# Kernel tuning notes

Hardware: AMD Instinct MI355X
Metric: run time of the kernel (lower is better)

The kernel has to match this reference:

```python
import jax, jax.numpy as jnp
import numpy as np

B, N, D_MODEL = 2, 4096, 2048
H = 4
KEY_DIM = 1024          # d_model * 0.5
DK = KEY_DIM // H       # 256, head_qk_dim
DV = D_MODEL // H       # 512, head_v_dim
CHUNK = 64
EPS = 1e-5


def setup_inputs() -> dict:
    key = jax.random.key(0)
    ks = jax.random.split(key, 6)
    s = 0.02  # small init scale, mimics xavier-ish magnitude
    return {
        "x": jax.random.normal(ks[0], (B, N, D_MODEL), jnp.float32),
        "Wq": jax.random.normal(ks[1], (KEY_DIM, D_MODEL), jnp.float32) * s,
        "Wk": jax.random.normal(ks[2], (KEY_DIM, D_MODEL), jnp.float32) * s,
        "Wv": jax.random.normal(ks[3], (D_MODEL, D_MODEL), jnp.float32) * s,
        "Wg": jax.random.normal(ks[4], (D_MODEL, D_MODEL), jnp.float32) * s,
        "Wo": jax.random.normal(ks[5], (D_MODEL, D_MODEL), jnp.float32) * s,
        "gnorm_w": jnp.ones((DV,), jnp.float32),
    }


def _rope(qk):
    # non-interleaved rotary over full head dim; qk: [b, n, h, d]
    n, d = qk.shape[1], qk.shape[3]
    inv_freq = 1.0 / (10000.0 ** (jnp.arange(0, d, 2, dtype=jnp.float32) / d))
    freqs = jnp.arange(n, dtype=jnp.float32)[:, None] * inv_freq[None, :]  # [n, d/2]
    cos = jnp.cos(freqs)[None, :, None, :]
    sin = jnp.sin(freqs)[None, :, None, :]
    x1, x2 = qk[..., : d // 2], qk[..., d // 2 :]
    return jnp.concatenate([x1 * cos - x2 * sin, x2 * cos + x1 * sin], axis=-1)


def _retention_forward(x, Wq, Wk, Wv, Wg, Wo, gnorm_w):
    b, n, dm = x.shape
    dk, dv = Wq.shape[0] // H, Wv.shape[0] // H
    q = (x @ Wq.T).reshape(b, n, H, dk)
    k = (x @ Wk.T).reshape(b, n, H, dk)
    q, k = _rope(q), _rope(k)
    v = (x @ Wv.T).reshape(b, n, H, dv)
    # -> [b, h, n, d]
    q = q.transpose(0, 2, 1, 3) * (dk ** -0.5)
    k = k.transpose(0, 2, 1, 3)
    v = v.transpose(0, 2, 1, 3)

    # multi-scale decay: gamma_h = 1 - 2^(-5-h)
    gamma = 1.0 - jnp.exp2(-5.0 - jnp.arange(H, dtype=jnp.float32))  # [H]

    C = CHUNK
    nc = n // C
    qc = q.reshape(b, H, nc, C, dk).transpose(2, 0, 1, 3, 4)  # [nc,b,H,C,dk]
    kc = k.reshape(b, H, nc, C, dk).transpose(2, 0, 1, 3, 4)
    vc = v.reshape(b, H, nc, C, dv).transpose(2, 0, 1, 3, 4)

    i = jnp.arange(C)
    expo = (i[:, None] - i[None, :]).astype(jnp.float32)          # i - j
    dmask = jnp.where(expo >= 0, gamma[:, None, None] ** expo, 0.0)  # [H,C,C]
    g_in = gamma[:, None] ** (i + 1).astype(jnp.float32)          # [H,C] cross-chunk decay
    g_k = gamma[:, None] ** (C - 1 - i).astype(jnp.float32)       # [H,C] state-update decay
    g_C = gamma ** C                                               # [H]

    def step(S, inp):
        qi, ki, vi = inp  # [b,H,C,dk], [b,H,C,dk], [b,H,C,dv]
        attn = jnp.einsum('bhid,bhjd->bhij', qi, ki) * dmask[None]
        o_intra = jnp.einsum('bhij,bhjv->bhiv', attn, vi)
        o_inter = jnp.einsum('bhid,bhdv->bhiv', qi, S) * g_in[None, :, :, None]
        S_new = S * g_C[None, :, None, None] + jnp.einsum(
            'bhjd,bhjv->bhdv', ki * g_k[None, :, :, None], vi)
        return S_new, o_intra + o_inter

    S0 = jnp.zeros((b, H, dk, dv), x.dtype)
    _, oc = jax.lax.scan(step, S0, (qc, kc, vc))          # oc: [nc,b,H,C,dv]
    o = oc.transpose(1, 0, 3, 2, 4).reshape(b, n, H, dv)  # [b,n,h,dv]

    # per-head RMSNorm (group_norm over head_v_dim)
    o = o * jax.lax.rsqrt(jnp.mean(o * o, axis=-1, keepdims=True) + EPS) * gnorm_w

    g = jax.nn.silu(x @ Wg.T)  # [b,n,d_model]
    return (o.reshape(b, n, H * dv) * g) @ Wo.T


def reference(x, Wq, Wk, Wv, Wg, Wo, gnorm_w):
    return _retention_forward(x, Wq, Wk, Wv, Wg, Wo, gnorm_w)
```

## Files before the change

### kernel.cpp

```cpp
#include <hip/hip_runtime.h>
#include <hip/hip_bf16.h>
#include <stdint.h>

constexpr int Bb   = 2;
constexpr int Nn   = 4096;
constexpr int DM   = 2048;
constexpr int Hh   = 4;
constexpr int DK   = 256;
constexpr int DV   = 512;
constexpr int QKS  = 2048;
constexpr int CH   = 64;
constexpr int NC   = Nn / CH;
constexpr int M    = Bb * Nn;

typedef __attribute__((ext_vector_type(8))) short s16x8;
typedef __attribute__((ext_vector_type(4))) float f32x4;

__device__ __forceinline__ float b2f(uint16_t h) {
  return __uint_as_float(((uint32_t)h) << 16);
}
__device__ __forceinline__ uint16_t f2b(float f) {
  uint32_t u = __float_as_uint(f);
  return (uint16_t)((u + 0x7fffu + ((u >> 16) & 1u)) >> 16);
}

__device__ __forceinline__ void gload16(const void* g, void* l) {
  __builtin_amdgcn_global_load_lds(
      (const __attribute__((address_space(1))) void*)g,
      (__attribute__((address_space(3))) void*)l, 16, 0, 0);
}

__global__ __launch_bounds__(256) void conv_f2b(const float* __restrict__ s,
                                                uint16_t* __restrict__ d, int n8) {
  int i = blockIdx.x * 256 + threadIdx.x;
  if (i >= n8) return;
  const float4* sp = (const float4*)s;
  float4 a = sp[2 * i], b = sp[2 * i + 1];
  uint4 o;
  o.x = (uint32_t)f2b(a.x) | ((uint32_t)f2b(a.y) << 16);
  o.y = (uint32_t)f2b(a.z) | ((uint32_t)f2b(a.w) << 16);
  o.z = (uint32_t)f2b(b.x) | ((uint32_t)f2b(b.y) << 16);
  o.w = (uint32_t)f2b(b.z) | ((uint32_t)f2b(b.w) << 16);
  ((uint4*)d)[i] = o;
}

__global__ __launch_bounds__(256) void conv_w4(const float* __restrict__ Wq,
                                               const float* __restrict__ Wk,
                                               const float* __restrict__ Wv,
                                               const float* __restrict__ Wg,
                                               uint16_t* __restrict__ dst) {
  const int i = blockIdx.x * 256 + threadIdx.x;
  const float* s; int off;
  if (i < 262144)       { s = Wq; off = i; }
  else if (i < 524288)  { s = Wk; off = i - 262144; }
  else if (i < 1048576) { s = Wv; off = i - 524288; }
  else                  { s = Wg; off = i - 1048576; }
  const float4* sp = (const float4*)s;
  float4 a = sp[2 * off], b = sp[2 * off + 1];
  uint4 o;
  o.x = (uint32_t)f2b(a.x) | ((uint32_t)f2b(a.y) << 16);
  o.y = (uint32_t)f2b(a.z) | ((uint32_t)f2b(a.w) << 16);
  o.z = (uint32_t)f2b(b.x) | ((uint32_t)f2b(b.y) << 16);
  o.w = (uint32_t)f2b(b.z) | ((uint32_t)f2b(b.w) << 16);
  ((uint4*)dst)[i] = o;
}

__global__ __launch_bounds__(512, 2) void gemm_fused3(const uint16_t* __restrict__ A,
                                                      const uint16_t* __restrict__ W,
                                                      uint16_t* __restrict__ out0,
                                                      int K) {
  __shared__ uint16_t As[3][256 * 32];
  __shared__ uint16_t Bs[3][256 * 32];
  const int tid = threadIdx.x;
  const int l = tid & 63, w = tid >> 6;
  const int wm = w >> 2, wn = w & 3;
  const int m0 = blockIdx.x * 256, n0 = blockIdx.y * 256;
  const int fr = l & 15, fk = (l >> 4) * 8;
  const int fkA = fk ^ ((fr & 3) << 3);
  const int sk = ((tid & 3) ^ ((tid >> 2) & 3)) * 8;
  const uint16_t* aP = A + (size_t)(m0 + w * 16 + (l >> 2)) * K + sk;
  const uint16_t* wP = W + (size_t)(n0 + w * 16 + (l >> 2)) * K + sk;

  f32x4 acc[8][4];
#pragma unroll
  for (int mi = 0; mi < 8; ++mi)
#pragma unroll
    for (int nj = 0; nj < 4; ++nj) {
      f32x4 z = {0.f, 0.f, 0.f, 0.f};
      acc[mi][nj] = z;
    }

#define STAGE256(T, BUF)                                                     \
  {                                                                          \
    const size_t k0_ = (size_t)(T) * 32;                                     \
    uint16_t* as_ = &As[BUF][w * 512];                                       \
    uint16_t* bs_ = &Bs[BUF][w * 512];                                       \
    gload16(aP + k0_, as_);                                                  \
    gload16(aP + (size_t)128 * K + k0_, as_ + 4096);                         \
    gload16(wP + k0_, bs_);                                                  \
    gload16(wP + (size_t)128 * K + k0_, bs_ + 4096);                         \
  }

  const int NT = K / 32;
  STAGE256(0, 0);
  STAGE256(1, 1);
  for (int t = 0; t < NT; ++t) {
    if (t < NT - 1) asm volatile("s_waitcnt vmcnt(4)" ::: "memory");
    else            asm volatile("s_waitcnt vmcnt(0)" ::: "memory");
    __builtin_amdgcn_s_barrier();
    __builtin_amdgcn_sched_barrier(0);
    if (t + 2 < NT) STAGE256(t + 2, (t + 2) % 3);
    const int cur = t % 3;
    s16x8 af[8], bf4[4];
    const uint16_t* Ab = &As[cur][(wm * 128 + fr) * 32 + fkA];
    const uint16_t* Bp = &Bs[cur][(wn * 64 + fr) * 32 + fkA];
#pragma unroll
    for (int mi = 0; mi < 8; ++mi) af[mi] = *(const s16x8*)(Ab + mi * 512);
#pragma unroll
    for (int nj = 0; nj < 4; ++nj) bf4[nj] = *(const s16x8*)(Bp + nj * 512);
    __builtin_amdgcn_s_setprio(1);
#pragma unroll
    for (int mi = 0; mi < 8; ++mi)
#pragma unroll
      for (int nj = 0; nj < 4; ++nj)
        acc[mi][nj] = __builtin_amdgcn_mfma_f32_16x16x32_bf16(af[mi], bf4[nj],
                                                              acc[mi][nj], 0, 0, 0);
    __builtin_amdgcn_s_setprio(0);
  }
#undef STAGE256

  uint16_t* Cb = out0 + (size_t)(n0 >> 11) * 16777216;
  const int r0 = m0 + wm * 128 + (l >> 4) * 4;
  const int c0 = (n0 & 2047) + wn * 64 + fr;
#pragma unroll
  for (int mi = 0; mi < 8; ++mi)
#pragma unroll
    for (int nj = 0; nj < 4; ++nj)
#pragma unroll
      for (int p = 0; p < 4; ++p) {
        const int row = r0 + mi * 16 + p;
        const int col = c0 + nj * 16;
        Cb[(size_t)row * 2048 + col] = f2b(acc[mi][nj][p]);
      }
}

__global__ __launch_bounds__(512, 2) void gemm_fin(const uint16_t* __restrict__ A,
                                                   const uint16_t* __restrict__ W,
                                                   float* __restrict__ C,
                                                   int Nd, int K) {
  __shared__ uint16_t As[3][256 * 32];
  __shared__ uint16_t Bs[3][128 * 32];
  const int tid = threadIdx.x;
  const int l = tid & 63, w = tid >> 6;
  const int wm = w >> 2, wn = w & 3;
  const int m0 = blockIdx.x * 256, n0 = blockIdx.y * 128;
  const int fr = l & 15, fk = (l >> 4) * 8;
  const int fkA = fk ^ ((fr & 3) << 3);
  const int sk = ((tid & 3) ^ ((tid >> 2) & 3)) * 8;
  const uint16_t* aP = A + (size_t)(m0 + w * 16 + (l >> 2)) * K + sk;
  const uint16_t* wP = W + (size_t)(n0 + w * 16 + (l >> 2)) * K + sk;

  f32x4 acc[8][2];
#pragma unroll
  for (int mi = 0; mi < 8; ++mi)
#pragma unroll
    for (int nj = 0; nj < 2; ++nj) {
      f32x4 z = {0.f, 0.f, 0.f, 0.f};
      acc[mi][nj] = z;
    }

#define STAGEF(T, BUF)                                                       \
  {                                                                          \
    const size_t k0_ = (size_t)(T) * 32;                                     \
    uint16_t* as_ = &As[BUF][w * 512];                                       \
    gload16(aP + k0_, as_);                                                  \
    gload16(aP + (size_t)128 * K + k0_, as_ + 4096);                         \
    gload16(wP + k0_, &Bs[BUF][w * 512]);                                    \
  }

  const int NT = K / 32;
  STAGEF(0, 0);
  STAGEF(1, 1);
  for (int t = 0; t < NT; ++t) {
    if (t < NT - 1) asm volatile("s_waitcnt vmcnt(3)" ::: "memory");
    else            asm volatile("s_waitcnt vmcnt(0)" ::: "memory");
    __builtin_amdgcn_s_barrier();
    __builtin_amdgcn_sched_barrier(0);
    if (t + 2 < NT) STAGEF(t + 2, (t + 2) % 3);
    const int cur = t % 3;
    s16x8 af[8], bf2[2];
    const uint16_t* Ab = &As[cur][(wm * 128 + fr) * 32 + fkA];
    const uint16_t* Bp = &Bs[cur][(wn * 32 + fr) * 32 + fkA];
#pragma unroll
    for (int mi = 0; mi < 8; ++mi) af[mi] = *(const s16x8*)(Ab + mi * 512);
#pragma unroll
    for (int nj = 0; nj < 2; ++nj) bf2[nj] = *(const s16x8*)(Bp + nj * 512);
    __builtin_amdgcn_s_setprio(1);
#pragma unroll
    for (int mi = 0; mi < 8; ++mi)
#pragma unroll
      for (int nj = 0; nj < 2; ++nj)
        acc[mi][nj] = __builtin_amdgcn_mfma_f32_16x16x32_bf16(af[mi], bf2[nj],
                                                              acc[mi][nj], 0, 0, 0);
    __builtin_amdgcn_s_setprio(0);
  }
#undef STAGEF

  const int r0 = m0 + wm * 128 + (l >> 4) * 4;
  const int c0 = n0 + wn * 32 + fr;
#pragma unroll
  for (int mi = 0; mi < 8; ++mi)
#pragma unroll
    for (int nj = 0; nj < 2; ++nj)
#pragma unroll
      for (int p = 0; p < 4; ++p)
        C[(size_t)(r0 + mi * 16 + p) * Nd + c0 + nj * 16] = acc[mi][nj][p];
}

__global__ void rope_kernel(uint16_t* __restrict__ qk) {
  const int idx = blockIdx.x * 256 + threadIdx.x;
  const int i = idx & 127;
  const int h = (idx >> 7) & 3;
  const int n = (idx >> 9) & (Nn - 1);
  const int b = idx >> 21;
  const size_t base = ((size_t)(b * Nn + n)) * QKS + h * DK;
  const float invf = (float)exp((double)i * -0.071955784156063938);
  const float theta = (float)n * invf;
  float sn, cs;
  sincosf(theta, &sn, &cs);
  float x1 = b2f(qk[base + i]), x2 = b2f(qk[base + 128 + i]);
  qk[base + i]       = f2b((x1 * cs - x2 * sn) * 0.0625f);
  qk[base + 128 + i] = f2b((x2 * cs + x1 * sn) * 0.0625f);
  x1 = b2f(qk[base + 1024 + i]); x2 = b2f(qk[base + 1024 + 128 + i]);
  qk[base + 1024 + i]       = f2b(x1 * cs - x2 * sn);
  qk[base + 1024 + 128 + i] = f2b(x2 * cs + x1 * sn);
}

__global__ __launch_bounds__(256) void transpose_v(const uint16_t* __restrict__ v,
                                                   uint16_t* __restrict__ vt) {
  const int nt = blockIdx.x & 63;
  const int wt = (blockIdx.x >> 6) & 7;
  const int bh = blockIdx.x >> 9;
  const int b = bh >> 2, h = bh & 3;
  __shared__ uint16_t t[64][72];
  const int lr = threadIdx.x >> 2, lc = (threadIdx.x & 3) * 16;
  const uint16_t* src = v + ((size_t)(b * Nn + nt * 64 + lr)) * DM + h * DV + wt * 64 + lc;
  *(uint4*)&t[lr][lc]     = *(const uint4*)src;
  *(uint4*)&t[lr][lc + 8] = *(const uint4*)(src + 8);
  __syncthreads();
  uint16_t out[16];
#pragma unroll
  for (int e = 0; e < 16; ++e) out[e] = t[lc + e][lr];
  uint16_t* dst = vt + ((size_t)bh * 512 + wt * 64 + lr) * 4096 + nt * 64 + lc;
  *(uint4*)dst       = *(uint4*)&out[0];
  *(uint4*)(dst + 8) = *(uint4*)&out[8];
}

__global__ __launch_bounds__(256) void transpose_k(const uint16_t* __restrict__ qk,
                                                   uint16_t* __restrict__ kt) {
  const int nt = blockIdx.x & 63;
  const int dt = (blockIdx.x >> 6) & 3;
  const int bh = blockIdx.x >> 8;
  const int b = bh >> 2, h = bh & 3;
  __shared__ uint16_t t[64][72];
  const int lr = threadIdx.x >> 2, lc = (threadIdx.x & 3) * 16;
  const uint16_t* src = qk + ((size_t)(b * Nn + nt * 64 + lr)) * QKS + 1024 + h * DK + dt * 64 + lc;
  *(uint4*)&t[lr][lc]     = *(const uint4*)src;
  *(uint4*)&t[lr][lc + 8] = *(const uint4*)(src + 8);
  __syncthreads();
  const float l2g = log2f(1.f - exp2f(-5.f - (float)h));
  uint16_t out[16];
#pragma unroll
  for (int e = 0; e < 16; ++e)
    out[e] = f2b(b2f(t[lc + e][lr]) * exp2f((float)(63 - (lc + e)) * l2g));
  uint16_t* dst = kt + ((size_t)bh * 256 + dt * 64 + lr) * 4096 + nt * 64 + lc;
  *(uint4*)dst       = *(uint4*)&out[0];
  *(uint4*)(dst + 8) = *(uint4*)&out[8];
}

__global__ __launch_bounds__(256) void attn_mfma(const uint16_t* __restrict__ qk,
                                                 uint16_t* __restrict__ attn) {
  const int c  = blockIdx.x & 63;
  const int bh = blockIdx.x >> 6;
  const int b = bh >> 2, h = bh & 3;
  const int tid = threadIdx.x;
  const int l = tid & 63, w = tid >> 6;
  const int fr = l & 15, fk = (l >> 4) * 8;
  const int n0 = c * CH;
  const uint16_t* qbase = qk + ((size_t)(b * Nn + n0)) * QKS + h * DK;
  const uint16_t* kbase = qbase + 1024;
  f32x4 acc[4];
#pragma unroll
  for (int nj = 0; nj < 4; ++nj) {
    f32x4 z = {0.f, 0.f, 0.f, 0.f};
    acc[nj] = z;
  }
#pragma unroll
  for (int ks = 0; ks < 8; ++ks) {
    s16x8 qf = *(const s16x8*)(qbase + (size_t)(w * 16 + fr) * QKS + ks * 32 + fk);
    s16x8 kf[4];
#pragma unroll
    for (int nj = 0; nj < 4; ++nj)
      kf[nj] = *(const s16x8*)(kbase + (size_t)(nj * 16 + fr) * QKS + ks * 32 + fk);
#pragma unroll
    for (int nj = 0; nj < 4; ++nj)
      acc[nj] = __builtin_amdgcn_mfma_f32_16x16x32_bf16(qf, kf[nj], acc[nj], 0, 0, 0);
  }
  const float l2g = log2f(1.f - exp2f(-5.f - (float)h));
  uint16_t* ab = attn + ((size_t)bh * 64 + c) * 4096;
  const int rbase = (l >> 4) * 4;
#pragma unroll
  for (int pp = 0; pp < 4; ++pp) {
    const int i = w * 16 + rbase + pp;
#pragma unroll
    for (int nj = 0; nj < 4; ++nj) {
      const int j = nj * 16 + fr;
      const float val = (i >= j) ? acc[nj][pp] * exp2f((float)(i - j) * l2g) : 0.f;
      ab[(size_t)i * 64 + j] = f2b(val);
    }
  }
}

__global__ __launch_bounds__(256) void chunk_outer(const uint16_t* __restrict__ kt,
                                                   const uint16_t* __restrict__ vt,
                                                   uint16_t* __restrict__ U, int p) {
  const int c  = blockIdx.x & 63;
  const int bh = blockIdx.x >> 6;
  const int tid = threadIdx.x;
  const int l = tid & 63, w = tid >> 6;
  const int wrow = (w >> 1) * 64;
  const int wcol = (w & 1) * 128;
  const int fr = l & 15, fk = (l >> 4) * 8;
  const int n0 = c * CH;
  const uint16_t* vtb = vt + ((size_t)bh * 512 + p * 128) * 4096 + n0;
  const uint16_t* ktb = kt + ((size_t)bh * 256) * 4096 + n0;
  f32x4 acc[4][8];
#pragma unroll
  for (int mi = 0; mi < 4; ++mi)
#pragma unroll
    for (int nj = 0; nj < 8; ++nj) {
      f32x4 z = {0.f, 0.f, 0.f, 0.f};
      acc[mi][nj] = z;
    }
#pragma unroll
  for (int ks = 0; ks < 2; ++ks) {
    s16x8 af[4], bf8[8];
#pragma unroll
    for (int mi = 0; mi < 4; ++mi)
      af[mi] = *(const s16x8*)(vtb + (size_t)(wrow + mi * 16 + fr) * 4096 + ks * 32 + fk);
#pragma unroll
    for (int nj = 0; nj < 8; ++nj)
      bf8[nj] = *(const s16x8*)(ktb + (size_t)(wcol + nj * 16 + fr) * 4096 + ks * 32 + fk);
#pragma unroll
    for (int mi = 0; mi < 4; ++mi)
#pragma unroll
      for (int nj = 0; nj < 8; ++nj)
        acc[mi][nj] = __builtin_amdgcn_mfma_f32_16x16x32_bf16(af[mi], bf8[nj],
                                                              acc[mi][nj], 0, 0, 0);
  }
  uint16_t* Ub = U + (size_t)bh * 2097152 + (size_t)c * 32768;
  const int rbase = (l >> 4) * 4;
#pragma unroll
  for (int mi = 0; mi < 4; ++mi)
#pragma unroll
    for (int nj = 0; nj < 8; ++nj)
#pragma unroll
      for (int pp = 0; pp < 4; ++pp) {
        const int wq = wrow + mi * 16 + rbase + pp;
        const int d  = wcol + nj * 16 + fr;
        Ub[(size_t)wq * 256 + d] = f2b(acc[mi][nj][pp]);
      }
}

__global__ __launch_bounds__(256) void state_scan(uint16_t* __restrict__ U) {
  const int gid = blockIdx.x * 256 + threadIdx.x;
  const int bh = gid >> 15;
  const int e  = gid & 32767;
  const int h  = bh & 3;
  const float l2g = log2f(1.f - exp2f(-5.f - (float)h));
  const float gC = exp2f(64.f * l2g);
  uint16_t* p = U + (size_t)bh * 2097152 + e;
  float S = 0.f;
  for (int cb = 0; cb < 8; ++cb) {
    uint16_t* base = p + (size_t)cb * 8 * 32768;
    float u[8];
#pragma unroll
    for (int ee = 0; ee < 8; ++ee) u[ee] = b2f(base[(size_t)ee * 32768]);
#pragma unroll
    for (int ee = 0; ee < 8; ++ee) {
      base[(size_t)ee * 32768] = f2b(S);
      S = gC * S + u[ee];
    }
  }
}

__global__ __launch_bounds__(256) void scan_out(const uint16_t* __restrict__ qk,
                                                const uint16_t* __restrict__ vt,
                                                const uint16_t* __restrict__ attn,
                                                const uint16_t* __restrict__ U,
                                                uint16_t* __restrict__ o, int p) {
  const int c  = blockIdx.x & 63;
  const int bh = blockIdx.x >> 6;
  const int b = bh >> 2, h = bh & 3;
  const int tid = threadIdx.x;
  const int l = tid & 63, wv = tid >> 6;
  const int wcol = wv * 32;
  const int fr = l & 15, fk = (l >> 4) * 8;
  const int n0 = c * CH;
  f32x4 aQS[4][2], aPV[4][2];
#pragma unroll
  for (int mi = 0; mi < 4; ++mi)
#pragma unroll
    for (int nj = 0; nj < 2; ++nj) {
      f32x4 z = {0.f, 0.f, 0.f, 0.f};
      aQS[mi][nj] = z; aPV[mi][nj] = z;
    }
  const uint16_t* qbase = qk + ((size_t)(b * Nn + n0)) * QKS + h * DK;
  const uint16_t* Ub = U + (size_t)bh * 2097152 + (size_t)c * 32768;
#pragma unroll
  for (int ks = 0; ks < 8; ++ks) {
    s16x8 qf[4], sf[2];
#pragma unroll
    for (int mi = 0; mi < 4; ++mi)
      qf[mi] = *(const s16x8*)(qbase + (size_t)(mi * 16 + fr) * QKS + ks * 32 + fk);
#pragma unroll
    for (int nj = 0; nj < 2; ++nj)
      sf[nj] = *(const s16x8*)(Ub + (size_t)(wcol + nj * 16 + fr) * 256 + ks * 32 + fk);
#pragma unroll
    for (int mi = 0; mi < 4; ++mi)
#pragma unroll
      for (int nj = 0; nj < 2; ++nj)
        aQS[mi][nj] = __builtin_amdgcn_mfma_f32_16x16x32_bf16(qf[mi], sf[nj],
                                                              aQS[mi][nj], 0, 0, 0);
  }
  const uint16_t* ab = attn + ((size_t)bh * 64 + c) * 4096;
  const uint16_t* vtb = vt + ((size_t)bh * 512 + p * 128) * 4096 + n0;
#pragma unroll
  for (int ks = 0; ks < 2; ++ks) {
    s16x8 af[4], vf[2];
#pragma unroll
    for (int mi = 0; mi < 4; ++mi)
      af[mi] = *(const s16x8*)(ab + (size_t)(mi * 16 + fr) * 64 + ks * 32 + fk);
#pragma unroll
    for (int nj = 0; nj < 2; ++nj)
      vf[nj] = *(const s16x8*)(vtb + (size_t)(wcol + nj * 16 + fr) * 4096 + ks * 32 + fk);
#pragma unroll
    for (int mi = 0; mi < 4; ++mi)
#pragma unroll
      for (int nj = 0; nj < 2; ++nj)
        aPV[mi][nj] = __builtin_amdgcn_mfma_f32_16x16x32_bf16(af[mi], vf[nj],
                                                              aPV[mi][nj], 0, 0, 0);
  }
  const float l2g = log2f(1.f - exp2f(-5.f - (float)h));
  const int rbase = (l >> 4) * 4;
#pragma unroll
  for (int mi = 0; mi < 4; ++mi)
#pragma unroll
    for (int pp = 0; pp < 4; ++pp) {
      const int i = mi * 16 + rbase + pp;
      const float gi = exp2f((float)(i + 1) * l2g);
#pragma unroll
      for (int nj = 0; nj < 2; ++nj) {
        const int wc_ = wcol + nj * 16 + fr;
        const float val = aPV[mi][nj][pp] + gi * aQS[mi][nj][pp];
        o[((size_t)(b * Nn + n0 + i)) * DM + h * DV + p * 128 + wc_] = f2b(val);
      }
    }
}

__global__ __launch_bounds__(256) void gn_gate(const uint16_t* __restrict__ o,
                                               uint16_t* __restrict__ g,
                                               const float* __restrict__ gw) {
  const int bn = blockIdx.x;
  const int tid = threadIdx.x;
  const int h = tid >> 6;
  const int lane = tid & 63;
  const size_t base = (size_t)bn * DM + h * DV + lane * 8;
  uint4 ov4 = *(const uint4*)&o[base];
  float ov[8] = { b2f((uint16_t)ov4.x), b2f((uint16_t)(ov4.x >> 16)),
                  b2f((uint16_t)ov4.y), b2f((uint16_t)(ov4.y >> 16)),
                  b2f((uint16_t)ov4.z), b2f((uint16_t)(ov4.z >> 16)),
                  b2f((uint16_t)ov4.w), b2f((uint16_t)(ov4.w >> 16)) };
  float ss = 0.f;
#pragma unroll
  for (int e = 0; e < 8; ++e) ss += ov[e] * ov[e];
#pragma unroll
  for (int m = 1; m < 64; m <<= 1) ss += __shfl_xor(ss, m, 64);
  const float r = rsqrtf(ss * (1.f / 512.f) + 1e-5f);
  uint4 gv = *(const uint4*)&g[base];
  float gf[8] = { b2f((uint16_t)gv.x), b2f((uint16_t)(gv.x >> 16)),
                  b2f((uint16_t)gv.y), b2f((uint16_t)(gv.y >> 16)),
                  b2f((uint16_t)gv.z), b2f((uint16_t)(gv.z >> 16)),
                  b2f((uint16_t)gv.w), b2f((uint16_t)(gv.w >> 16)) };
  const float* gwp = gw + lane * 8;
  uint16_t res[8];
#pragma unroll
  for (int e = 0; e < 8; ++e) {
    float sil = gf[e] / (1.f + expf(-gf[e]));
    res[e] = f2b(ov[e] * r * gwp[e] * sil);
  }
  uint4 outv;
  outv.x = (uint32_t)res[0] | ((uint32_t)res[1] << 16);
  outv.y = (uint32_t)res[2] | ((uint32_t)res[3] << 16);
  outv.z = (uint32_t)res[4] | ((uint32_t)res[5] << 16);
  outv.w = (uint32_t)res[6] | ((uint32_t)res[7] << 16);
  *(uint4*)&g[base] = outv;
}

extern "C" void kernel_launch(void* const* d_in, const int* in_sizes, int n_in,
                              void* d_out, int out_size, void* d_ws, size_t ws_size,
                              hipStream_t stream) {
  const float* x  = (const float*)d_in[0];
  const float* Wq = (const float*)d_in[1];
  const float* Wk = (const float*)d_in[2];
  const float* Wv = (const float*)d_in[3];
  const float* Wg = (const float*)d_in[4];
  const float* Wo = (const float*)d_in[5];
  const float* gw = (const float*)d_in[6];

  char* base = (char*)d_ws;
  uint16_t* xb   = (uint16_t*)(base);
  uint16_t* U    = (uint16_t*)(base);
  uint16_t* qkb  = (uint16_t*)(base + ((size_t)32 << 20));
  uint16_t* vb   = (uint16_t*)(base + ((size_t)64 << 20));
  uint16_t* kt   = (uint16_t*)(base + ((size_t)64 << 20));
  uint16_t* attn = (uint16_t*)(base + ((size_t)80 << 20));
  uint16_t* wob  = (uint16_t*)(base + ((size_t)84 << 20));
  uint16_t* gb   = (uint16_t*)(base + ((size_t)96 << 20));
  uint16_t* wall = (uint16_t*)(base + ((size_t)128 << 20));
  uint16_t* vt   = (uint16_t*)(base + ((size_t)128 << 20));
  uint16_t* qb   = qkb;
  uint16_t* o16  = (uint16_t*)d_out;

  dim3 blk(256), blkG(512);
  conv_f2b<<<dim3(8192), blk, 0, stream>>>(x, xb, M * DM / 8);
  conv_w4<<<dim3(6144), blk, 0, stream>>>(Wq, Wk, Wv, Wg, wall);
  gemm_fused3<<<dim3(M/256, 6144/256), blkG, 0, stream>>>(xb, wall, qkb, DM);
  rope_kernel<<<dim3((Bb*Nn*Hh*128)/256), blk, 0, stream>>>(qkb);
  transpose_v<<<dim3(8*8*64), blk, 0, stream>>>(vb, vt);
  conv_f2b<<<dim3(2048), blk, 0, stream>>>(Wo, wob, DM * DM / 8);
  transpose_k<<<dim3(8*4*64), blk, 0, stream>>>(qkb, kt);
  attn_mfma<<<dim3(Bb*Hh*NC), blk, 0, stream>>>(qkb, attn);
  for (int p = 0; p < 4; ++p) {
    chunk_outer<<<dim3(Bb*Hh*NC),  blk, 0, stream>>>(kt, vt, U, p);
    state_scan<<<dim3(1024),       blk, 0, stream>>>(U);
    scan_out<<<dim3(Bb*Hh*NC),     blk, 0, stream>>>(qb, vt, attn, U, o16, p);
  }
  gn_gate<<<dim3(M), blk, 0, stream>>>(o16, gb, gw);
  gemm_fin<<<dim3(M/256, DM/128), blkG, 0, stream>>>(gb, wob, (float*)d_out, DM, DM);
}
```

Before: 614.1 us.

## Restructure fused QKVG GEMM into fine-grained 8-wave ping-pong pipeline

Rewrites the main loop of the fused projection GEMM. A triple-buffered 32-wide K pipeline is replaced by a double-buffered 64-wide K scheme, split into half-tiles, with many barriers per iteration. Global-to-LDS loads are interleaved between MFMA quarter-blocks, and the LDS swizzle and staging layout are changed. The aim is to overlap memory traffic with matrix math more tightly. The cost is many extra barriers, and dropping the occupancy hint of 2 blocks may change register allocation.

Result: faster. 549.0 us (-10.6%).

```diff
diff --git a/kernel.cpp b/kernel.cpp
--- a/kernel.cpp
+++ b/kernel.cpp
@@ -29,6 +29,12 @@
       (const __attribute__((address_space(1))) void*)g,
       (__attribute__((address_space(3))) void*)l, 16, 0, 0);
 }
+
+#define BARRIER()  asm volatile("s_barrier" ::: "memory")
+#define WAITLGKM() do { asm volatile("s_waitcnt lgkmcnt(0)" ::: "memory"); \
+                        __builtin_amdgcn_sched_barrier(0); } while (0)
+#define VMCNT4()   asm volatile("s_waitcnt vmcnt(4)" ::: "memory")
+#define VMCNT0()   asm volatile("s_waitcnt vmcnt(0)" ::: "memory")
 
 __global__ __launch_bounds__(256) void conv_f2b(const float* __restrict__ s,
                                                 uint16_t* __restrict__ d, int n8) {
@@ -65,21 +71,21 @@
   ((uint4*)dst)[i] = o;
 }
 
-__global__ __launch_bounds__(512, 2) void gemm_fused3(const uint16_t* __restrict__ A,
-                                                      const uint16_t* __restrict__ W,
-                                                      uint16_t* __restrict__ out0,
-                                                      int K) {
-  __shared__ uint16_t As[3][256 * 32];
-  __shared__ uint16_t Bs[3][256 * 32];
+__global__ __launch_bounds__(512) void gemm_fused3(const uint16_t* __restrict__ A,
+                                                   const uint16_t* __restrict__ W,
+                                                   uint16_t* __restrict__ out0,
+                                                   int K) {
+  __shared__ uint16_t Al[2][2][8192];
+  __shared__ uint16_t Bl[2][2][8192];
   const int tid = threadIdx.x;
   const int l = tid & 63, w = tid >> 6;
   const int wm = w >> 2, wn = w & 3;
   const int m0 = blockIdx.x * 256, n0 = blockIdx.y * 256;
-  const int fr = l & 15, fk = (l >> 4) * 8;
-  const int fkA = fk ^ ((fr & 3) << 3);
-  const int sk = ((tid & 3) ^ ((tid >> 2) & 3)) * 8;
-  const uint16_t* aP = A + (size_t)(m0 + w * 16 + (l >> 2)) * K + sk;
-  const uint16_t* wP = W + (size_t)(n0 + w * 16 + (l >> 2)) * K + sk;
+  const int fr = l & 15;
+  const int pu = (((l >> 4) ^ ((fr >> 1) & 3)) * 8);
+  const int ssw = ((l & 3) ^ ((l >> 3) & 3)) * 8;
+  const uint16_t* aS = A + (size_t)(m0 + w * 32 + (l >> 2)) * K + ssw;
+  const uint16_t* wS = W + (size_t)(n0 + w * 32 + (l >> 2)) * K + ssw;
 
   f32x4 acc[8][4];
 #pragma unroll
@@ -90,44 +96,84 @@
       acc[mi][nj] = z;
     }
 
-#define STAGE256(T, BUF)                                                     \
-  {                                                                          \
-    const size_t k0_ = (size_t)(T) * 32;                                     \
-    uint16_t* as_ = &As[BUF][w * 512];                                       \
-    uint16_t* bs_ = &Bs[BUF][w * 512];                                       \
-    gload16(aP + k0_, as_);                                                  \
-    gload16(aP + (size_t)128 * K + k0_, as_ + 4096);                         \
-    gload16(wP + k0_, bs_);                                                  \
-    gload16(wP + (size_t)128 * K + k0_, bs_ + 4096);                         \
-  }
-
-  const int NT = K / 32;
-  STAGE256(0, 0);
-  STAGE256(1, 1);
-  for (int t = 0; t < NT; ++t) {
-    if (t < NT - 1) asm volatile("s_waitcnt vmcnt(4)" ::: "memory");
-    else            asm volatile("s_waitcnt vmcnt(0)" ::: "memory");
-    __builtin_amdgcn_s_barrier();
-    __builtin_amdgcn_sched_barrier(0);
-    if (t + 2 < NT) STAGE256(t + 2, (t + 2) % 3);
-    const int cur = t % 3;
-    s16x8 af[8], bf4[4];
-    const uint16_t* Ab = &As[cur][(wm * 128 + fr) * 32 + fkA];
-    const uint16_t* Bp = &Bs[cur][(wn * 64 + fr) * 32 + fkA];
-#pragma unroll
-    for (int mi = 0; mi < 8; ++mi) af[mi] = *(const s16x8*)(Ab + mi * 512);
-#pragma unroll
-    for (int nj = 0; nj < 4; ++nj) bf4[nj] = *(const s16x8*)(Bp + nj * 512);
-    __builtin_amdgcn_s_setprio(1);
-#pragma unroll
-    for (int mi = 0; mi < 8; ++mi)
-#pragma unroll
-      for (int nj = 0; nj < 4; ++nj)
-        acc[mi][nj] = __builtin_amdgcn_mfma_f32_16x16x32_bf16(af[mi], bf4[nj],
-                                                              acc[mi][nj], 0, 0, 0);
-    __builtin_amdgcn_s_setprio(0);
-  }
-#undef STAGE256
+#define STG_A(S, KH, KT) do {                                                \
+    const uint16_t* _p = aS + (size_t)(KT) * 64 + (KH) * 32;                 \
+    gload16(_p,                   &Al[S][KH][(w * 32) * 32]);                \
+    gload16(_p + (size_t)16 * K,  &Al[S][KH][(w * 32 + 16) * 32]);           \
+  } while (0)
+#define STG_B(S, KH, KT) do {                                                \
+    const uint16_t* _p = wS + (size_t)(KT) * 64 + (KH) * 32;                 \
+    gload16(_p,                   &Bl[S][KH][(w * 32) * 32]);                \
+    gload16(_p + (size_t)16 * K,  &Bl[S][KH][(w * 32 + 16) * 32]);           \
+  } while (0)
+#define LDA(S, KH, MI) (*(const s16x8*)&Al[S][KH][(wm * 128 + (MI) * 16 + fr) * 32 + pu])
+#define LDB(S, KH, NJ) (*(const s16x8*)&Bl[S][KH][(wn * 64 + (NJ) * 16 + fr) * 32 + pu])
+#define MFMA16(Q) do {                                                       \
+    __builtin_amdgcn_s_setprio(1);                                           \
+    _Pragma("unroll")                                                        \
+    for (int mi = 0; mi < 8; ++mi)                                           \
+      acc[mi][2*(Q)] = __builtin_amdgcn_mfma_f32_16x16x32_bf16(              \
+          aF[mi], bF0, acc[mi][2*(Q)], 0, 0, 0);                             \
+    _Pragma("unroll")                                                        \
+    for (int mi = 0; mi < 8; ++mi)                                           \
+      acc[mi][2*(Q)+1] = __builtin_amdgcn_mfma_f32_16x16x32_bf16(            \
+          aF[mi], bF1, acc[mi][2*(Q)+1], 0, 0, 0);                           \
+    __builtin_amdgcn_s_setprio(0);                                           \
+  } while (0)
+
+  STG_A(0, 0, 0); STG_B(0, 0, 0); STG_A(0, 1, 0); STG_B(0, 1, 0);
+  STG_A(1, 0, 1); STG_B(1, 0, 1);
+  VMCNT0();
+  BARRIER();
+
+  const int NI = K / 128;
+  s16x8 aF[8], bF0, bF1;
+
+  for (int i = 0; i < NI; ++i) {
+    const bool nl = (i < NI - 1);
+    const size_t t1 = 2 * i + 1, t2 = 2 * i + 2, t3 = 2 * i + 3;
+#pragma unroll
+    for (int mi = 0; mi < 8; ++mi) aF[mi] = LDA(0, 0, mi);
+    bF0 = LDB(0, 0, 0); bF1 = LDB(0, 0, 1);
+    STG_A(1, 1, t1);
+    BARRIER(); WAITLGKM(); MFMA16(0); BARRIER();
+    bF0 = LDB(0, 0, 2); bF1 = LDB(0, 0, 3);
+    STG_B(1, 1, t1);
+    BARRIER(); WAITLGKM(); MFMA16(1); BARRIER();
+#pragma unroll
+    for (int mi = 0; mi < 8; ++mi) aF[mi] = LDA(0, 1, mi);
+    bF0 = LDB(0, 1, 0); bF1 = LDB(0, 1, 1);
+    if (nl) STG_A(0, 0, t2);
+    BARRIER(); WAITLGKM(); MFMA16(0); BARRIER();
+    bF0 = LDB(0, 1, 2); bF1 = LDB(0, 1, 3);
+    if (nl) STG_B(0, 0, t2);
+    BARRIER(); WAITLGKM(); MFMA16(1);
+    if (nl) VMCNT4(); else VMCNT0();
+    BARRIER();
+#pragma unroll
+    for (int mi = 0; mi < 8; ++mi) aF[mi] = LDA(1, 0, mi);
+    bF0 = LDB(1, 0, 0); bF1 = LDB(1, 0, 1);
+    if (nl) STG_A(0, 1, t2);
+    BARRIER(); WAITLGKM(); MFMA16(0); BARRIER();
+    bF0 = LDB(1, 0, 2); bF1 = LDB(1, 0, 3);
+    if (nl) STG_B(0, 1, t2);
+    BARRIER(); WAITLGKM(); MFMA16(1); BARRIER();
+#pragma unroll
+    for (int mi = 0; mi < 8; ++mi) aF[mi] = LDA(1, 1, mi);
+    bF0 = LDB(1, 1, 0); bF1 = LDB(1, 1, 1);
+    if (nl) STG_A(1, 0, t3);
+    BARRIER(); WAITLGKM(); MFMA16(0); BARRIER();
+    bF0 = LDB(1, 1, 2); bF1 = LDB(1, 1, 3);
+    if (nl) STG_B(1, 0, t3);
+    BARRIER(); WAITLGKM(); MFMA16(1);
+    VMCNT4();
+    BARRIER();
+  }
+#undef STG_A
+#undef STG_B
+#undef LDA
+#undef LDB
+#undef MFMA16
 
   uint16_t* Cb = out0 + (size_t)(n0 >> 11) * 16777216;
   const int r0 = m0 + wm * 128 + (l >> 4) * 4;
```
